# Kernel optimization log

Hardware: AMD Instinct MI355X
Metric: run time of the kernel (lower is better)

## Reference

```python
import jax, jax.numpy as jnp
import numpy as np
from jax import lax

MAX_DECAY = 0.99
EPS = 1e-05
TOPK = 4


def ema_mask_group(moving_avg, new, mask, decay0, cluster_update_num):
    """Faithful port of ema_tensor_mask_group_inplace, including the quirk that
    the Python-level `decay` variable is carried (and possibly shrunk) across
    cluster iterations. Implemented as a lax.scan over clusters carrying decay.
    moving_avg/new: [C] or [C, D]; mask, cluster_update_num: [C].
    """
    def step(decay, xs):
        ma, nw, m, c = xs
        d = jnp.where((m != 0) & (c <= 10.0), decay * c / 10.0, decay)
        out = jnp.where(m != 0, ma * d + nw * (1.0 - d), ma)
        return d, out
    _, out = lax.scan(step, jnp.asarray(decay0, moving_avg.dtype),
                      (moving_avg, new, mask, cluster_update_num))
    return out


def laplace_smoothing(x, n_categories, eps=EPS):
    return (x + eps) / (x.sum() + n_categories * eps)


def setup_inputs() -> dict:
    key = jax.random.key(0)
    k1, k2 = jax.random.split(key)
    N, C, D = 65536, 512, 256
    return {
        "inputs_flatten": jax.random.normal(k1, (N, D), dtype=jnp.float32),
        "dictionary": jax.random.normal(k2, (C, D), dtype=jnp.float32),
        "cluster_size_sum": jnp.zeros((C,), dtype=jnp.float32),
        "cluster_value": jnp.zeros((C, D), dtype=jnp.float32),
        "cluster_update_num": jnp.ones((C,), dtype=jnp.float32),
    }


def reference(inputs_flatten, dictionary, cluster_size_sum, cluster_value,
              cluster_update_num):
    N, D = inputs_flatten.shape
    C = dictionary.shape[0]
    dic = lax.stop_gradient(dictionary)  # dictionary used via .detach()/.data

    # squared euclidean distances [N, C]
    distances = (jnp.sum(inputs_flatten ** 2, axis=1, keepdims=True)
                 + jnp.sum(dic ** 2, axis=1)
                 - 2.0 * jnp.matmul(inputs_flatten, dic.T))

    # ascending sort -> take topK smallest distances
    _, topk_idx = lax.top_k(-distances, TOPK)          # [N, K]
    topk_emb = dic[topk_idx]                            # [N, K, D]
    group_emb = jnp.sum(topk_emb, axis=1) / TOPK        # [N, D]

    # multi-hot encodings via scatter
    rows = jnp.arange(N)[:, None]
    encodings = jnp.zeros((N, C), dtype=jnp.float32).at[rows, topk_idx].set(1.0)

    # ---- training-mode EMA codebook update (single device: all_gather = identity) ----
    x_sg = lax.stop_gradient(inputs_flatten)
    cluster_size = jnp.sum(encodings, axis=0)           # [C]
    cluster_mask = (cluster_size != 0).astype(jnp.float32)
    cluster_update_num_new = cluster_update_num + cluster_mask

    cluster_size_sum_new = ema_mask_group(cluster_size_sum, cluster_size,
                                          cluster_mask, MAX_DECAY,
                                          cluster_update_num_new)
    input_sum = jnp.matmul(encodings.T, x_sg)           # [C, D]
    cluster_value_new = ema_mask_group(cluster_value, input_sum, cluster_mask,
                                       MAX_DECAY, cluster_update_num_new)

    cs = laplace_smoothing(cluster_size_sum_new, C, EPS) * cluster_size_sum_new.sum()
    embed_normalized = jnp.where(cluster_mask[:, None] == 1.0,
                                 cluster_value_new / cs[:, None],
                                 cluster_value_new)
    dictionary_new = embed_normalized                   # world_size == 1

    # straight-through estimator
    group_emb = lax.stop_gradient(group_emb - inputs_flatten) + inputs_flatten
    return (group_emb, topk_idx, dictionary_new, cluster_size_sum_new,
            cluster_value_new, cluster_update_num_new)
```

## Files before the change

kernel.cpp:

```cpp
#include <hip/hip_runtime.h>

#define N_ROWS 65536
#define C_CLUST 512
#define D_DIM 256

#define WS_DICTT   0
#define WS_DSQ     131072
#define WS_XSQ     131584
#define WS_CS      197120
#define WS_DCY     197632
#define WS_ISUM    198144
#define WS_COUNTS  329216
#define WS_OFFSETS 329728
#define WS_FILL    330752
#define WS_ROWLIST 331264

#define OUT_GEMB 0
#define OUT_TOPK 16777216
#define OUT_DICT 17039360
#define OUT_CSS  17170432
#define OUT_CV   17170944
#define OUT_CNUM 17302016

#define RPB 128

typedef __attribute__((ext_vector_type(8))) short short8;
typedef __attribute__((ext_vector_type(16))) float f32x16;

__device__ __forceinline__ unsigned short f2bf(float v) {
    union { float f; unsigned u; } c; c.f = v;
    unsigned r = c.u + 0x7FFFu + ((c.u >> 16) & 1u);
    return (unsigned short)(r >> 16);
}
__device__ __forceinline__ float bf2f(unsigned short h) {
    union { float f; unsigned u; } c; c.u = ((unsigned)h) << 16;
    return c.f;
}

__global__ void zero_k(unsigned* counts, unsigned* fill, float* isum) {
    int t = blockIdx.x * blockDim.x + threadIdx.x;
    if (t < 512) { counts[t] = 0u; fill[t] = 0u; }
    if (t < C_CLUST * D_DIM) isum[t] = 0.f;
}

__global__ void prep_dict(const float* __restrict__ dic, float* __restrict__ ws) {
    int c = blockIdx.x, k = threadIdx.x;
    float v = dic[c * D_DIM + k];
    unsigned short* dhi = (unsigned short*)(ws + WS_DICTT);
    unsigned short* dlo = dhi + 131072;
    unsigned short hb = f2bf(v);
    dhi[c * D_DIM + k] = hb;
    dlo[c * D_DIM + k] = f2bf(__fsub_rn(v, bf2f(hb)));
    __shared__ float red[256];
    red[k] = v * v;
    __syncthreads();
    for (int s = 128; s > 0; s >>= 1) {
        if (k < s) red[k] += red[k + s];
        __syncthreads();
    }
    if (k == 0) ws[WS_DSQ + c] = red[0];
}

__global__ void row_sq(const float* __restrict__ x, float* __restrict__ ws) {
    int row = blockIdx.x, k = threadIdx.x;
    float v = x[row * D_DIM + k];
    __shared__ float red[256];
    red[k] = v * v;
    __syncthreads();
    for (int s = 128; s > 0; s >>= 1) {
        if (k < s) red[k] += red[k + s];
        __syncthreads();
    }
    if (k == 0) ws[WS_XSQ + row] = red[0];
}

__global__ __launch_bounds__(256, 2) void stage1_cand(
    const float* __restrict__ x, const float* __restrict__ ws,
    float* __restrict__ cand_out)
{
    __shared__ unsigned short hlds[32 * 264];
    __shared__ unsigned short llds[32 * 264];
    __shared__ float dsq_s[512];

    const int tid = threadIdx.x;
    const int lane = tid & 63;
    const int w = tid >> 6;
    const int kg = lane >> 5;
    const int cl_lane = lane & 31;
    const int row = blockIdx.x * 128 + w * 32 + cl_lane;

    const unsigned short* dhi = (const unsigned short*)(ws + WS_DICTT);
    const unsigned short* dlo = dhi + 131072;

    for (int i = tid; i < 512; i += 256) dsq_s[i] = ws[WS_DSQ + i];

    short8 bhi[16], blo[16];
    #pragma unroll
    for (int s = 0; s < 16; ++s) {
        const float* px = &x[(size_t)row * D_DIM + s * 16 + kg * 8];
        float4 u0 = *reinterpret_cast<const float4*>(px);
        float4 u1 = *reinterpret_cast<const float4*>(px + 4);
        float vv[8] = {u0.x, u0.y, u0.z, u0.w, u1.x, u1.y, u1.z, u1.w};
        short8 h, l;
        #pragma unroll
        for (int e = 0; e < 8; ++e) {
            unsigned short hb = f2bf(vv[e]);
            unsigned short lb = f2bf(__fsub_rn(vv[e], bf2f(hb)));
            h[e] = (short)hb; l[e] = (short)lb;
        }
        bhi[s] = h; blo[s] = l;
    }

    unsigned long long kk[8];
    #pragma unroll
    for (int q = 0; q < 8; ++q) kk[q] = 0xFFFFFFFFFFFFFFFFULL;

    for (int ct = 0; ct < 16; ++ct) {
        __syncthreads();
        for (int q = tid; q < 1024; q += 256) {
            int c = q >> 5, k8 = (q & 31) * 8;
            *reinterpret_cast<uint4*>(&hlds[c * 264 + k8]) =
                *reinterpret_cast<const uint4*>(&dhi[(ct * 32 + c) * D_DIM + k8]);
            *reinterpret_cast<uint4*>(&llds[c * 264 + k8]) =
                *reinterpret_cast<const uint4*>(&dlo[(ct * 32 + c) * D_DIM + k8]);
        }
        __syncthreads();

        f32x16 ahh, ahl, alh;
        #pragma unroll
        for (int r = 0; r < 16; ++r) { ahh[r] = 0.f; ahl[r] = 0.f; alh[r] = 0.f; }

        #pragma unroll
        for (int s = 0; s < 16; ++s) {
            short8 Ah = *reinterpret_cast<const short8*>(
                &hlds[cl_lane * 264 + s * 16 + kg * 8]);
            short8 Al = *reinterpret_cast<const short8*>(
                &llds[cl_lane * 264 + s * 16 + kg * 8]);
            ahh = __builtin_amdgcn_mfma_f32_32x32x16_bf16(Ah, bhi[s], ahh, 0, 0, 0);
            ahl = __builtin_amdgcn_mfma_f32_32x32x16_bf16(Ah, blo[s], ahl, 0, 0, 0);
            alh = __builtin_amdgcn_mfma_f32_32x32x16_bf16(Al, bhi[s], alh, 0, 0, 0);
        }

        #pragma unroll
        for (int r = 0; r < 16; ++r) {
            int cl = ct * 32 + (r & 3) + 8 * (r >> 2) + 4 * kg;
            float dot = ahh[r] + ahl[r] + alh[r];
            float key = (dsq_s[cl] + 1024.0f) - 2.0f * dot;
            unsigned long long v =
                ((unsigned long long)__float_as_uint(key) << 32) | (unsigned)cl;
            #pragma unroll
            for (int q = 0; q < 8; ++q) {
                bool lt = v < kk[q];
                unsigned long long mn = lt ? v : kk[q];
                unsigned long long mx = lt ? kk[q] : v;
                kk[q] = mn; v = mx;
            }
        }
    }

    uint4 wv;
    wv.x = (unsigned)(kk[0] & 0xFFFF) | ((unsigned)(kk[1] & 0xFFFF) << 16);
    wv.y = (unsigned)(kk[2] & 0xFFFF) | ((unsigned)(kk[3] & 0xFFFF) << 16);
    wv.z = (unsigned)(kk[4] & 0xFFFF) | ((unsigned)(kk[5] & 0xFFFF) << 16);
    wv.w = (unsigned)(kk[6] & 0xFFFF) | ((unsigned)(kk[7] & 0xFFFF) << 16);
    *reinterpret_cast<uint4*>(&cand_out[(size_t)row * 256 + kg * 4]) = wv;
}

__global__ __launch_bounds__(256, 4) void refine_k(
    const float* __restrict__ x, const float* __restrict__ dic,
    const float* __restrict__ ws, float* __restrict__ out,
    unsigned* __restrict__ counts)
{
    __shared__ float xl[16 * 260];
    __shared__ float distb[256];
    __shared__ int cidx[256];
    __shared__ int seli[16 * 4];

    const int t = threadIdx.x;
    const int rowBase = blockIdx.x * 16;
    const unsigned short* candp = (const unsigned short*)(out + OUT_GEMB);

    cidx[t] = (int)candp[(size_t)(rowBase + (t >> 4)) * 512 + (t & 15)];

    #pragma unroll
    for (int i = 0; i < 4; ++i) {
        int q = t + i * 256;
        int r = q >> 6, seg = q & 63;
        *reinterpret_cast<float4*>(&xl[r * 260 + seg * 4]) =
            *reinterpret_cast<const float4*>(
                &x[(size_t)(rowBase + r) * D_DIM + seg * 4]);
    }
    __syncthreads();

    {
        int r = t >> 4;
        int ci = cidx[t];
        const float* dp = &dic[(size_t)ci * D_DIM];
        const float* xp = &xl[r * 260];
        float acc = 0.f;
        #pragma unroll 8
        for (int k4 = 0; k4 < 64; ++k4) {
            float4 dv = *reinterpret_cast<const float4*>(dp + k4 * 4);
            float4 xv = *reinterpret_cast<const float4*>(xp + k4 * 4);
            acc = fmaf(xv.x, dv.x, acc);
            acc = fmaf(xv.y, dv.y, acc);
            acc = fmaf(xv.z, dv.z, acc);
            acc = fmaf(xv.w, dv.w, acc);
        }
        float ds = ws[WS_DSQ + ci];
        float xs = ws[WS_XSQ + rowBase + r];
        distb[t] = __fsub_rn(__fadd_rn(xs, ds), __fmul_rn(2.0f, acc));
    }
    __syncthreads();

    if (t < 16) {
        float bv0 = 3.4e38f, bv1 = 3.4e38f, bv2 = 3.4e38f, bv3 = 3.4e38f;
        int bi0 = 0x7FFFFFFF, bi1 = 0x7FFFFFFF, bi2 = 0x7FFFFFFF, bi3 = 0x7FFFFFFF;
        for (int s = 0; s < 16; ++s) {
            int p = t * 16 + s;
            float v = distb[p];
            int ci = cidx[p];
            if (v < bv3 || (v == bv3 && ci < bi3)) {
                if (v < bv2 || (v == bv2 && ci < bi2)) {
                    bv3 = bv2; bi3 = bi2;
                    if (v < bv1 || (v == bv1 && ci < bi1)) {
                        bv2 = bv1; bi2 = bi1;
                        if (v < bv0 || (v == bv0 && ci < bi0)) {
                            bv1 = bv0; bi1 = bi0;
                            bv0 = v; bi0 = ci;
                        } else { bv1 = v; bi1 = ci; }
                    } else { bv2 = v; bi2 = ci; }
                } else { bv3 = v; bi3 = ci; }
            }
        }
        int row = rowBase + t;
        out[OUT_TOPK + (size_t)row * 4 + 0] = (float)bi0;
        out[OUT_TOPK + (size_t)row * 4 + 1] = (float)bi1;
        out[OUT_TOPK + (size_t)row * 4 + 2] = (float)bi2;
        out[OUT_TOPK + (size_t)row * 4 + 3] = (float)bi3;
        atomicAdd(&counts[bi0], 1u);
        atomicAdd(&counts[bi1], 1u);
        atomicAdd(&counts[bi2], 1u);
        atomicAdd(&counts[bi3], 1u);
        seli[t * 4 + 0] = bi0;
        seli[t * 4 + 1] = bi1;
        seli[t * 4 + 2] = bi2;
        seli[t * 4 + 3] = bi3;
    }
    __syncthreads();

    {
        int r = t >> 4, u = t & 15;
        int p0 = seli[r * 4 + 0], p1 = seli[r * 4 + 1];
        int p2 = seli[r * 4 + 2], p3 = seli[r * 4 + 3];
        #pragma unroll
        for (int h = 0; h < 4; ++h) {
            int k4 = u * 16 + h * 4;
            float4 a = *reinterpret_cast<const float4*>(&dic[(size_t)p0 * D_DIM + k4]);
            float4 b = *reinterpret_cast<const float4*>(&dic[(size_t)p1 * D_DIM + k4]);
            float4 c = *reinterpret_cast<const float4*>(&dic[(size_t)p2 * D_DIM + k4]);
            float4 e = *reinterpret_cast<const float4*>(&dic[(size_t)p3 * D_DIM + k4]);
            float4 xv = *reinterpret_cast<const float4*>(&xl[r * 260 + k4]);
            float4 o;
            float g;
            g = __fmul_rn(__fadd_rn(__fadd_rn(__fadd_rn(a.x, b.x), c.x), e.x), 0.25f);
            o.x = __fadd_rn(__fsub_rn(g, xv.x), xv.x);
            g = __fmul_rn(__fadd_rn(__fadd_rn(__fadd_rn(a.y, b.y), c.y), e.y), 0.25f);
            o.y = __fadd_rn(__fsub_rn(g, xv.y), xv.y);
            g = __fmul_rn(__fadd_rn(__fadd_rn(__fadd_rn(a.z, b.z), c.z), e.z), 0.25f);
            o.z = __fadd_rn(__fsub_rn(g, xv.z), xv.z);
            g = __fmul_rn(__fadd_rn(__fadd_rn(__fadd_rn(a.w, b.w), c.w), e.w), 0.25f);
            o.w = __fadd_rn(__fsub_rn(g, xv.w), xv.w);
            *reinterpret_cast<float4*>(
                &out[OUT_GEMB + (size_t)(rowBase + r) * D_DIM + k4]) = o;
        }
    }
}

__global__ void prefix_k(const unsigned* __restrict__ counts, unsigned* __restrict__ offsets) {
    __shared__ unsigned s[512];
    int t = threadIdx.x;
    unsigned my = counts[t];
    s[t] = my;
    __syncthreads();
    for (int off = 1; off < 512; off <<= 1) {
        unsigned v = (t >= off) ? s[t - off] : 0u;
        __syncthreads();
        s[t] += v;
        __syncthreads();
    }
    offsets[t] = s[t] - my;
    if (t == 511) offsets[512] = s[511];
}

__global__ void scatter_k(const float* __restrict__ topk, const unsigned* __restrict__ offsets,
                          unsigned* __restrict__ fill, unsigned* __restrict__ rowlist) {
    int row = blockIdx.x * 256 + threadIdx.x;
    #pragma unroll
    for (int k = 0; k < 4; ++k) {
        int c = (int)topk[row * 4 + k];
        unsigned p = atomicAdd(&fill[c], 1u);
        rowlist[offsets[c] + p] = ((unsigned)c << 16) | (unsigned)row;
    }
}

__global__ __launch_bounds__(256, 8) void cluster_sum2_k(
    const float* __restrict__ x, const unsigned* __restrict__ rowlist,
    float* __restrict__ isum)
{
    const int d = threadIdx.x;
    const int base = blockIdx.x * RPB;
    unsigned e0 = rowlist[base];
    int ccur = (int)(e0 >> 16);
    float acc = 0.f;
    #pragma unroll 4
    for (int j = 0; j < RPB; ++j) {
        unsigned e = rowlist[base + j];
        int c = (int)(e >> 16);
        float v = x[(e & 0xFFFFu) * D_DIM + d];
        if (c != ccur) {
            atomicAdd(&isum[ccur * D_DIM + d], acc);
            acc = 0.f;
            ccur = c;
        }
        acc += v;
    }
    atomicAdd(&isum[ccur * D_DIM + d], acc);
}

__global__ void ema_scalar_k(const float* __restrict__ css_in, const float* __restrict__ cnum_in,
                             const unsigned* __restrict__ counts,
                             float* __restrict__ ws, float* __restrict__ out) {
    __shared__ float sdecay[512];
    __shared__ float sred[512];
    __shared__ float scn[512];
    __shared__ unsigned smask[512];
    int t = threadIdx.x;
    unsigned cnt = counts[t];
    float size = (float)cnt;
    float mask = (cnt != 0u) ? 1.f : 0.f;
    float cnum_new = __fadd_rn(cnum_in[t], mask);
    scn[t] = cnum_new;
    smask[t] = cnt;
    __syncthreads();
    if (t == 0) {
        float d = 0.99f;
        for (int c = 0; c < 512; ++c) {
            if (smask[c] != 0u && scn[c] <= 10.0f)
                d = __fmul_rn(d, scn[c]) / 10.0f;
            sdecay[c] = d;
        }
    }
    __syncthreads();
    float d = sdecay[t];
    float css = css_in[t];
    float css_new = (cnt != 0u)
        ? __fadd_rn(__fmul_rn(css, d), __fmul_rn(size, __fsub_rn(1.f, d)))
        : css;
    out[OUT_CSS + t] = css_new;
    out[OUT_CNUM + t] = cnum_new;
    sred[t] = css_new;
    __syncthreads();
    for (int s = 256; s > 0; s >>= 1) {
        if (t < s) sred[t] += sred[t + s];
        __syncthreads();
    }
    float S = sred[0];
    float cs = __fmul_rn(__fdiv_rn(__fadd_rn(css_new, 1e-5f),
                                   __fadd_rn(S, 0.00512f)), S);
    ws[WS_CS + t] = cs;
    ws[WS_DCY + t] = d;
}

__global__ void final_k(const float* __restrict__ cv_in, const float* __restrict__ ws,
                        const unsigned* __restrict__ counts, float* __restrict__ out) {
    int c = blockIdx.x, d = threadIdx.x;
    float isum = ws[WS_ISUM + c * D_DIM + d];
    float dc = ws[WS_DCY + c];
    float cs = ws[WS_CS + c];
    unsigned cnt = counts[c];
    float cv = cv_in[c * D_DIM + d];
    float cvn = (cnt != 0u)
        ? __fadd_rn(__fmul_rn(cv, dc), __fmul_rn(isum, __fsub_rn(1.f, dc)))
        : cv;
    out[OUT_CV + c * D_DIM + d] = cvn;
    out[OUT_DICT + c * D_DIM + d] = (cnt != 0u) ? __fdiv_rn(cvn, cs) : cvn;
}

extern "C" void kernel_launch(void* const* d_in, const int* in_sizes, int n_in,
                              void* d_out, int out_size, void* d_ws, size_t ws_size,
                              hipStream_t stream) {
    const float* x       = (const float*)d_in[0];
    const float* dic     = (const float*)d_in[1];
    const float* css_in  = (const float*)d_in[2];
    const float* cv_in   = (const float*)d_in[3];
    const float* cnum_in = (const float*)d_in[4];
    float* out = (float*)d_out;
    float* ws  = (float*)d_ws;
    unsigned* counts  = (unsigned*)(ws + WS_COUNTS);
    unsigned* offsets = (unsigned*)(ws + WS_OFFSETS);
    unsigned* fill    = (unsigned*)(ws + WS_FILL);
    unsigned* rowlist = (unsigned*)(ws + WS_ROWLIST);

    zero_k<<<C_CLUST * D_DIM / 256, 256, 0, stream>>>(counts, fill, ws + WS_ISUM);
    prep_dict<<<C_CLUST, 256, 0, stream>>>(dic, ws);
    row_sq<<<N_ROWS, 256, 0, stream>>>(x, ws);

    stage1_cand<<<N_ROWS / 128, 256, 0, stream>>>(x, ws, out + OUT_GEMB);

    refine_k<<<N_ROWS / 16, 256, 0, stream>>>(x, dic, ws, out, counts);

    prefix_k<<<1, 512, 0, stream>>>(counts, offsets);
    scatter_k<<<N_ROWS / 256, 256, 0, stream>>>(out + OUT_TOPK, offsets, fill, rowlist);
    cluster_sum2_k<<<N_ROWS * 4 / RPB, 256, 0, stream>>>(x, rowlist, ws + WS_ISUM);
    ema_scalar_k<<<1, 512, 0, stream>>>(css_in, cnum_in, counts, ws, out);
    final_k<<<C_CLUST, 256, 0, stream>>>(cv_in, ws, counts, out);
}
```

Before: 649.4 us.

## Stage candidate dictionary rows through LDS and split group-emb into separate kernel

The refine kernel now loads the 16 candidate dictionary rows per query in coalesced 16-float chunks into a padded shared-memory tile. Previously each thread read its own 1 KB dictionary row with strided per-thread loads. The group-embedding computation moves out of refine_k into a new kernel that reads top-k indices back from global memory, which shrinks refine_k's shared memory and tail work. The cost is an extra launch, rereading x and the indices from global memory, and 32 added barriers per block in the refine loop. The larger dstage buffer also raises LDS use and may lower occupancy.

```diff
diff --git a/kernel.cpp b/kernel.cpp
--- a/kernel.cpp
+++ b/kernel.cpp
@@ -172,9 +172,9 @@
     unsigned* __restrict__ counts)
 {
     __shared__ float xl[16 * 260];
+    __shared__ float dstage[256 * 17];
     __shared__ float distb[256];
     __shared__ int cidx[256];
-    __shared__ int seli[16 * 4];
 
     const int t = threadIdx.x;
     const int rowBase = blockIdx.x * 16;
@@ -192,21 +192,38 @@
     }
     __syncthreads();
 
+    const float* dbase[4];
+    int spair[4], sf4[4];
+    #pragma unroll
+    for (int i = 0; i < 4; ++i) {
+        int q = t + i * 256;
+        spair[i] = q >> 2;
+        sf4[i] = q & 3;
+        dbase[i] = &dic[(size_t)cidx[spair[i]] * D_DIM + sf4[i] * 4];
+    }
+
+    const int r = t >> 4;
+    const float* xp = &xl[r * 260];
+    float acc = 0.f;
+
+    for (int chunk = 0; chunk < 16; ++chunk) {
+        #pragma unroll
+        for (int i = 0; i < 4; ++i) {
+            float4 dv = *reinterpret_cast<const float4*>(dbase[i] + chunk * 16);
+            float* dst = &dstage[spair[i] * 17 + sf4[i] * 4];
+            dst[0] = dv.x; dst[1] = dv.y; dst[2] = dv.z; dst[3] = dv.w;
+        }
+        __syncthreads();
+        const float* dp = &dstage[t * 17];
+        const float* xc = xp + chunk * 16;
+        #pragma unroll
+        for (int k = 0; k < 16; ++k)
+            acc = fmaf(xc[k], dp[k], acc);
+        __syncthreads();
+    }
+
     {
-        int r = t >> 4;
         int ci = cidx[t];
-        const float* dp = &dic[(size_t)ci * D_DIM];
-        const float* xp = &xl[r * 260];
-        float acc = 0.f;
-        #pragma unroll 8
-        for (int k4 = 0; k4 < 64; ++k4) {
-            float4 dv = *reinterpret_cast<const float4*>(dp + k4 * 4);
-            float4 xv = *reinterpret_cast<const float4*>(xp + k4 * 4);
-            acc = fmaf(xv.x, dv.x, acc);
-            acc = fmaf(xv.y, dv.y, acc);
-            acc = fmaf(xv.z, dv.z, acc);
-            acc = fmaf(xv.w, dv.w, acc);
-        }
         float ds = ws[WS_DSQ + ci];
         float xs = ws[WS_XSQ + rowBase + r];
         distb[t] = __fsub_rn(__fadd_rn(xs, ds), __fmul_rn(2.0f, acc));
@@ -242,39 +259,36 @@
         atomicAdd(&counts[bi1], 1u);
         atomicAdd(&counts[bi2], 1u);
         atomicAdd(&counts[bi3], 1u);
-        seli[t * 4 + 0] = bi0;
-        seli[t * 4 + 1] = bi1;
-        seli[t * 4 + 2] = bi2;
-        seli[t * 4 + 3] = bi3;
-    }
-    __syncthreads();
-
-    {
-        int r = t >> 4, u = t & 15;
-        int p0 = seli[r * 4 + 0], p1 = seli[r * 4 + 1];
-        int p2 = seli[r * 4 + 2], p3 = seli[r * 4 + 3];
-        #pragma unroll
-        for (int h = 0; h < 4; ++h) {
-            int k4 = u * 16 + h * 4;
-            float4 a = *reinterpret_cast<const float4*>(&dic[(size_t)p0 * D_DIM + k4]);
-            float4 b = *reinterpret_cast<const float4*>(&dic[(size_t)p1 * D_DIM + k4]);
-            float4 c = *reinterpret_cast<const float4*>(&dic[(size_t)p2 * D_DIM + k4]);
-            float4 e = *reinterpret_cast<const float4*>(&dic[(size_t)p3 * D_DIM + k4]);
-            float4 xv = *reinterpret_cast<const float4*>(&xl[r * 260 + k4]);
-            float4 o;
-            float g;
-            g = __fmul_rn(__fadd_rn(__fadd_rn(__fadd_rn(a.x, b.x), c.x), e.x), 0.25f);
-            o.x = __fadd_rn(__fsub_rn(g, xv.x), xv.x);
-            g = __fmul_rn(__fadd_rn(__fadd_rn(__fadd_rn(a.y, b.y), c.y), e.y), 0.25f);
-            o.y = __fadd_rn(__fsub_rn(g, xv.y), xv.y);
-            g = __fmul_rn(__fadd_rn(__fadd_rn(__fadd_rn(a.z, b.z), c.z), e.z), 0.25f);
-            o.z = __fadd_rn(__fsub_rn(g, xv.z), xv.z);
-            g = __fmul_rn(__fadd_rn(__fadd_rn(__fadd_rn(a.w, b.w), c.w), e.w), 0.25f);
-            o.w = __fadd_rn(__fsub_rn(g, xv.w), xv.w);
-            *reinterpret_cast<float4*>(
-                &out[OUT_GEMB + (size_t)(rowBase + r) * D_DIM + k4]) = o;
-        }
-    }
+    }
+}
+
+__global__ __launch_bounds__(256, 4) void group_emb_k(
+    const float* __restrict__ x, const float* __restrict__ dic,
+    const float* __restrict__ topk, float* __restrict__ out)
+{
+    const int t = threadIdx.x;
+    const int row = blockIdx.x * 4 + (t >> 6);
+    const int k4 = (t & 63) * 4;
+    int i0 = (int)topk[(size_t)row * 4 + 0];
+    int i1 = (int)topk[(size_t)row * 4 + 1];
+    int i2 = (int)topk[(size_t)row * 4 + 2];
+    int i3 = (int)topk[(size_t)row * 4 + 3];
+    float4 a = *reinterpret_cast<const float4*>(&dic[(size_t)i0 * D_DIM + k4]);
+    float4 b = *reinterpret_cast<const float4*>(&dic[(size_t)i1 * D_DIM + k4]);
+    float4 c = *reinterpret_cast<const float4*>(&dic[(size_t)i2 * D_DIM + k4]);
+    float4 e = *reinterpret_cast<const float4*>(&dic[(size_t)i3 * D_DIM + k4]);
+    float4 xv = *reinterpret_cast<const float4*>(&x[(size_t)row * D_DIM + k4]);
+    float4 o;
+    float g;
+    g = __fmul_rn(__fadd_rn(__fadd_rn(__fadd_rn(a.x, b.x), c.x), e.x), 0.25f);
+    o.x = __fadd_rn(__fsub_rn(g, xv.x), xv.x);
+    g = __fmul_rn(__fadd_rn(__fadd_rn(__fadd_rn(a.y, b.y), c.y), e.y), 0.25f);
+    o.y = __fadd_rn(__fsub_rn(g, xv.y), xv.y);
+    g = __fmul_rn(__fadd_rn(__fadd_rn(__fadd_rn(a.z, b.z), c.z), e.z), 0.25f);
+    o.z = __fadd_rn(__fsub_rn(g, xv.z), xv.z);
+    g = __fmul_rn(__fadd_rn(__fadd_rn(__fadd_rn(a.w, b.w), c.w), e.w), 0.25f);
+    o.w = __fadd_rn(__fsub_rn(g, xv.w), xv.w);
+    *reinterpret_cast<float4*>(&out[OUT_GEMB + (size_t)row * D_DIM + k4]) = o;
 }
 
 __global__ void prefix_k(const unsigned* __restrict__ counts, unsigned* __restrict__ offsets) {
@@ -409,6 +423,7 @@
     stage1_cand<<<N_ROWS / 128, 256, 0, stream>>>(x, ws, out + OUT_GEMB);
 
     refine_k<<<N_ROWS / 16, 256, 0, stream>>>(x, dic, ws, out, counts);
+    group_emb_k<<<N_ROWS / 4, 256, 0, stream>>>(x, dic, out + OUT_TOPK, out + OUT_GEMB);
 
     prefix_k<<<1, 512, 0, stream>>>(counts, offsets);
     scatter_k<<<N_ROWS / 256, 256, 0, stream>>>(out + OUT_TOPK, offsets, fill, rowlist);
```

New measurement: 651.1 us. No clear change (+0.3%).
